# Kernel optimization log

Measured on AMD Instinct MI355X. Metric: run time of the kernel, lower is better.

Reference implementation:

```python
import jax, jax.numpy as jnp
import numpy as np

B, T, E = 2, 2048, 1024
H, D = 16, 64          # num_heads, head_dim (v_head_dim == head_dim)


def setup_inputs() -> dict:
    key = jax.random.key(0)
    ks = jax.random.split(key, 10)
    s = lambda fan_in: 1.0 / np.sqrt(fan_in)
    inp = {
        "embed": jax.random.normal(ks[0], (B, T, E), dtype=jnp.float32),
        "mask": jax.random.randint(ks[1], (B, T, T), 0, 2) > 0,
        # Linear weights stored as [in, out] (y = x @ W + b)
        "Wq": jax.random.uniform(ks[2], (E, H * D), minval=-s(E), maxval=s(E)),
        "bq": jnp.zeros((H * D,), jnp.float32),
        "Wk": jax.random.uniform(ks[3], (E, H * D), minval=-s(E), maxval=s(E)),
        "bk": jnp.zeros((H * D,), jnp.float32),
        "Wv": jax.random.uniform(ks[4], (E, H * D), minval=-s(E), maxval=s(E)),
        "bv": jnp.zeros((H * D,), jnp.float32),
        "Wz": jax.random.uniform(ks[5], (H * D, E), minval=-s(H * D), maxval=s(H * D)),
        "bz": jnp.zeros((E,), jnp.float32),
    }
    return inp


def reference(embed, mask, Wq, bq, Wk, bk, Wv, bv, Wz, bz):
    # Self-attention: context = embed
    q = (embed @ Wq + bq).reshape(B, T, H, D)   # b t h d
    k = (embed @ Wk + bk).reshape(B, T, H, D)   # b T h d
    v = (embed @ Wv + bv).reshape(B, T, H, D)   # b T h d

    scale = D ** (-0.5)
    score = jnp.einsum('bthd,bThd->bhtT', q, k) * scale   # [b,h,t,T] materialized, as in source
    max_neg = -jnp.finfo(score.dtype).max
    score = jnp.where(mask[:, None, :, :], score, max_neg)
    norm_score = jax.nn.softmax(score, axis=-1)
    z = jnp.einsum('bhtT,bThd->bthd', norm_score, v)      # [b,t,h,d]
    flat_z = z.reshape(B, T, H * D)
    return flat_z @ Wz + bz
```

## Files before the change

kernel.cpp:

```cpp
#include <hip/hip_runtime.h>
#include <hip/hip_bf16.h>


typedef __bf16 bf8_t  __attribute__((ext_vector_type(8)));
typedef __bf16 bf4_t  __attribute__((ext_vector_type(4)));
typedef float  f4_t   __attribute__((ext_vector_type(4)));

constexpr int Bb = 2, Tt = 2048, Hh = 16, Dd = 64;

#define ASYNC16(g, l)                                                        \
    __builtin_amdgcn_global_load_lds(                                        \
        (const __attribute__((address_space(1))) void*)(g),                  \
        (__attribute__((address_space(3))) void*)(l), 16, 0, 0)

#if __has_builtin(__builtin_amdgcn_exp2f)
#define EXP2F(x) __builtin_amdgcn_exp2f(x)
#else
#define EXP2F(x) exp2f(x)
#endif

__global__ __launch_bounds__(256) void prep_kernel(
    const float* __restrict__ embed, const int* __restrict__ mask,
    const float* __restrict__ w0, const float* __restrict__ w1,
    const float* __restrict__ w2, const float* __restrict__ w3,
    __bf16* __restrict__ o0, __bf16* __restrict__ o1,
    __bf16* __restrict__ o2, __bf16* __restrict__ o3,
    __bf16* __restrict__ Eb, unsigned* __restrict__ Mbits)
{
    int z = blockIdx.x;
    if (z < 4096) {
        const float* in; __bf16* out;
        switch (z >> 10) {
            case 0: in = w0; out = o0; break;
            case 1: in = w1; out = o1; break;
            case 2: in = w2; out = o2; break;
            default: in = w3; out = o3; break;
        }
        int rem = z & 1023;
        int bx = (rem & 31) * 32;
        int by = (rem >> 5) * 32;
        __shared__ float t[32][33];
        int x  = threadIdx.x & 31;
        int y0 = threadIdx.x >> 5;
        #pragma unroll
        for (int i = 0; i < 4; i++) {
            int y = y0 + i * 8;
            t[y][x] = in[(size_t)(by + y) * 1024 + bx + x];
        }
        __syncthreads();
        #pragma unroll
        for (int i = 0; i < 4; i++) {
            int y = y0 + i * 8;
            out[(size_t)(bx + y) * 1024 + by + x] = (__bf16)t[x][y];
        }
    } else if (z < 5120) {
        size_t base = (size_t)(z - 4096) * 4096;
        #pragma unroll
        for (int j = 0; j < 4; j++) {
            size_t i = base + j * 1024 + threadIdx.x * 4;
            float4 v = *reinterpret_cast<const float4*>(embed + i);
            bf4_t o = {(__bf16)v.x, (__bf16)v.y, (__bf16)v.z, (__bf16)v.w};
            *reinterpret_cast<bf4_t*>(Eb + i) = o;
        }
    } else {
        size_t g = (size_t)(z - 5120) * 256 + threadIdx.x;
        const int* mp = mask + g * 32;
        unsigned v = 0;
        #pragma unroll
        for (int i = 0; i < 8; i++) {
            int4 m4 = *reinterpret_cast<const int4*>(mp + i * 4);
            if (m4.x) v |= 1u << (i * 4 + 0);
            if (m4.y) v |= 1u << (i * 4 + 1);
            if (m4.z) v |= 1u << (i * 4 + 2);
            if (m4.w) v |= 1u << (i * 4 + 3);
        }
        Mbits[g] = v;
    }
}

template <int TM, typename OutT>
__device__ __forceinline__ void gemm_body(const __bf16* __restrict__ A,
                                          const __bf16* __restrict__ Bt,
                                          const float* __restrict__ bias,
                                          OutT* __restrict__ out,
                                          int mode, float oscale, int bx, int by)
{
    constexpr int NI = TM / 32;
    alignas(16) __shared__ __bf16 As[TM * 64];
    alignas(16) __shared__ __bf16 Bs[128 * 64];

    int tid  = threadIdx.x;
    int lane = tid & 63;
    int quad = lane >> 4;
    int l16  = lane & 15;
    int wave = tid >> 6;
    int wm   = wave >> 1, wn = wave & 1;

    f4_t acc[NI][4];
    #pragma unroll
    for (int i = 0; i < NI; i++)
        #pragma unroll
        for (int j = 0; j < 4; j++)
            acc[i][j] = f4_t{0.f, 0.f, 0.f, 0.f};

    for (int kt = 0; kt < 1024; kt += 64) {
        #pragma unroll
        for (int i = 0; i < TM / 32; i++) {
            int c   = tid + 256 * i;
            int row = c >> 3, j = c & 7;
            ASYNC16(A + (size_t)(by * TM + row) * 1024 + kt + ((j ^ (row & 7)) * 8),
                    &As[c * 8]);
        }
        #pragma unroll
        for (int i = 0; i < 4; i++) {
            int c   = tid + 256 * i;
            int row = c >> 3, j = c & 7;
            ASYNC16(Bt + (size_t)(bx * 128 + row) * 1024 + kt + ((j ^ (row & 7)) * 8),
                    &Bs[c * 8]);
        }
        __syncthreads();

        bf8_t af[2][NI], bfr[2][4];
        #pragma unroll
        for (int c = 0; c < 2; c++) {
            #pragma unroll
            for (int im = 0; im < NI; im++) {
                int row = wm * (TM / 2) + im * 16 + l16;
                af[c][im] = *reinterpret_cast<const bf8_t*>(
                    &As[row * 64 + (((c * 4 + quad) ^ (row & 7)) * 8)]);
            }
            #pragma unroll
            for (int in_ = 0; in_ < 4; in_++) {
                int row = wn * 64 + in_ * 16 + l16;
                bfr[c][in_] = *reinterpret_cast<const bf8_t*>(
                    &Bs[row * 64 + (((c * 4 + quad) ^ (row & 7)) * 8)]);
            }
        }
        #pragma unroll
        for (int c = 0; c < 2; c++)
            #pragma unroll
            for (int im = 0; im < NI; im++)
                #pragma unroll
                for (int in_ = 0; in_ < 4; in_++)
                    acc[im][in_] = __builtin_amdgcn_mfma_f32_16x16x32_bf16(
                        af[c][im], bfr[c][in_], acc[im][in_], 0, 0, 0);
        __syncthreads();
    }

    #pragma unroll
    for (int im = 0; im < NI; im++) {
        #pragma unroll
        for (int in_ = 0; in_ < 4; in_++) {
            int gc  = bx * 128 + wn * 64 + in_ * 16 + l16;
            float bb = bias[gc];
            int gr0 = by * TM + wm * (TM / 2) + im * 16 + quad * 4;
            if (mode == 2) {
                int b = gr0 >> 11, t0 = gr0 & 2047;
                int h = gc >> 6,  d = gc & 63;
                bf4_t ov;
                #pragma unroll
                for (int r = 0; r < 4; r++)
                    ov[r] = (__bf16)(acc[im][in_][r] + bb);
                *reinterpret_cast<bf4_t*>(
                    (__bf16*)out + ((size_t)(b * Hh + h) * Dd + d) * Tt + t0) = ov;
            } else {
                #pragma unroll
                for (int r = 0; r < 4; r++) {
                    int gr  = gr0 + r;
                    float v = (acc[im][in_][r] + bb) * oscale;
                    size_t idx;
                    if (mode == 0) {
                        idx = (size_t)gr * 1024 + gc;
                    } else {
                        int b = gr >> 11, t = gr & 2047;
                        int h = gc >> 6,  d = gc & 63;
                        idx = ((size_t)(b * Hh + h) * Tt + t) * Dd + d;
                    }
                    out[idx] = (OutT)v;
                }
            }
        }
    }
}

__global__ __launch_bounds__(256) void gemm_qkv_kernel(
    const __bf16* __restrict__ A,
    const __bf16* __restrict__ WqT, const __bf16* __restrict__ WkT, const __bf16* __restrict__ WvT,
    const float* __restrict__ bq,  const float* __restrict__ bk,  const float* __restrict__ bv,
    __bf16* __restrict__ Qo, __bf16* __restrict__ Ko, __bf16* __restrict__ Vo)
{
    const __bf16* Bt; const float* bias; __bf16* out; int mode; float sc;
    if      (blockIdx.z == 0) { Bt = WqT; bias = bq; out = Qo; mode = 1; sc = 0.18033688011112042f; }
    else if (blockIdx.z == 1) { Bt = WkT; bias = bk; out = Ko; mode = 1; sc = 1.f; }
    else                      { Bt = WvT; bias = bv; out = Vo; mode = 2; sc = 1.f; }
    gemm_body<128, __bf16>(A, Bt, bias, out, mode, sc, blockIdx.x, blockIdx.y);
}

__global__ __launch_bounds__(256) void gemm_out_kernel(
    const __bf16* __restrict__ A, const __bf16* __restrict__ Bt,
    const float* __restrict__ bias, float* __restrict__ out)
{
    alignas(16) __shared__ __bf16 As[64 * 64];
    alignas(16) __shared__ __bf16 Bs[64 * 64];

    int tid  = threadIdx.x;
    int lane = tid & 63;
    int quad = lane >> 4;
    int l16  = lane & 15;
    int wave = tid >> 6;
    int wm   = wave >> 1, wn = wave & 1;
    int bx = blockIdx.x, by = blockIdx.y;

    f4_t acc[2][2];
    #pragma unroll
    for (int i = 0; i < 2; i++)
        #pragma unroll
        for (int j = 0; j < 2; j++)
            acc[i][j] = f4_t{0.f, 0.f, 0.f, 0.f};

    for (int kt = 0; kt < 1024; kt += 64) {
        #pragma unroll
        for (int i = 0; i < 2; i++) {
            int c   = tid + 256 * i;
            int row = c >> 3, j = c & 7;
            ASYNC16(A + (size_t)(by * 64 + row) * 1024 + kt + ((j ^ (row & 7)) * 8),
                    &As[c * 8]);
        }
        #pragma unroll
        for (int i = 0; i < 2; i++) {
            int c   = tid + 256 * i;
            int row = c >> 3, j = c & 7;
            ASYNC16(Bt + (size_t)(bx * 64 + row) * 1024 + kt + ((j ^ (row & 7)) * 8),
                    &Bs[c * 8]);
        }
        __syncthreads();

        bf8_t af[2][2], bfr[2][2];
        #pragma unroll
        for (int c = 0; c < 2; c++) {
            #pragma unroll
            for (int im = 0; im < 2; im++) {
                int row = wm * 32 + im * 16 + l16;
                af[c][im] = *reinterpret_cast<const bf8_t*>(
                    &As[row * 64 + (((c * 4 + quad) ^ (row & 7)) * 8)]);
            }
            #pragma unroll
            for (int in_ = 0; in_ < 2; in_++) {
                int row = wn * 32 + in_ * 16 + l16;
                bfr[c][in_] = *reinterpret_cast<const bf8_t*>(
                    &Bs[row * 64 + (((c * 4 + quad) ^ (row & 7)) * 8)]);
            }
        }
        #pragma unroll
        for (int c = 0; c < 2; c++)
            #pragma unroll
            for (int im = 0; im < 2; im++)
                #pragma unroll
                for (int in_ = 0; in_ < 2; in_++)
                    acc[im][in_] = __builtin_amdgcn_mfma_f32_16x16x32_bf16(
                        af[c][im], bfr[c][in_], acc[im][in_], 0, 0, 0);
        __syncthreads();
    }

    #pragma unroll
    for (int im = 0; im < 2; im++) {
        #pragma unroll
        for (int in_ = 0; in_ < 2; in_++) {
            int gc  = bx * 64 + wn * 32 + in_ * 16 + l16;
            float bb = bias[gc];
            int gr0 = by * 64 + wm * 32 + im * 16 + quad * 4;
            #pragma unroll
            for (int r = 0; r < 4; r++)
                out[(size_t)(gr0 + r) * 1024 + gc] = acc[im][in_][r] + bb;
        }
    }
}

__global__ __launch_bounds__(512, 4) void flash_kernel(
    const __bf16* __restrict__ Qb, const __bf16* __restrict__ Kb,
    const __bf16* __restrict__ Vb, const unsigned* __restrict__ Mbits,
    __bf16* __restrict__ Zb)
{
    alignas(16) __shared__ __bf16 Ks[2][64 * 64];
    alignas(16) __shared__ __bf16 Vs[2][64 * 64];
    alignas(16) __shared__ __bf16 Ps[8 * 16 * 72];

    int tid  = threadIdx.x;
    int lane = tid & 63;
    int wave = tid >> 6;
    int quad = lane >> 4;
    int l16  = lane & 15;
    int b = blockIdx.z, h = blockIdx.y;
    int bh = b * Hh + h;
    int qrow = blockIdx.x * 128 + wave * 16;

    int srow = tid >> 3, sj = tid & 7;
    const __bf16* kgp = Kb + ((size_t)bh * Tt + srow) * Dd + ((sj ^ (srow & 7)) * 8);
    const __bf16* vgp = Vb + ((size_t)bh * Dd + srow) * Tt + ((sj ^ (srow & 7)) * 8);
    const int sdst = tid * 8;

    bf8_t qf[2];
    #pragma unroll
    for (int c = 0; c < 2; c++)
        qf[c] = *reinterpret_cast<const bf8_t*>(
            Qb + ((size_t)bh * Tt + qrow + l16) * Dd + c * 32 + quad * 8);

    bf8_t ones;
    #pragma unroll
    for (int i = 0; i < 8; i++) ones[i] = (__bf16)1.0f;

    const unsigned* bmp = Mbits + ((size_t)b * Tt + qrow + l16) * 64;

    f4_t lacc = f4_t{0.f, 0.f, 0.f, 0.f};
    f4_t o[4];
    #pragma unroll
    for (int d = 0; d < 4; d++) o[d] = f4_t{0.f, 0.f, 0.f, 0.f};

    __bf16* pw = Ps + wave * 16 * 72;

    bf8_t kreg = *reinterpret_cast<const bf8_t*>(kgp);
    bf8_t vreg = *reinterpret_cast<const bf8_t*>(vgp);
    unsigned long long mreg = *reinterpret_cast<const unsigned long long*>(bmp);

    for (int kt = 0; kt < Tt; kt += 64) {
        int par = (kt >> 6) & 1;
        *reinterpret_cast<bf8_t*>(&Ks[par][sdst]) = kreg;
        *reinterpret_cast<bf8_t*>(&Vs[par][sdst]) = vreg;
        unsigned nib[4];
        #pragma unroll
        for (int n = 0; n < 4; n++)
            nib[n] = (unsigned)(mreg >> (n * 16 + quad * 4)) & 0xFu;
        __syncthreads();

        int ktn = (kt + 64 < Tt) ? kt + 64 : 0;
        kreg = *reinterpret_cast<const bf8_t*>(kgp + (size_t)ktn * Dd);
        vreg = *reinterpret_cast<const bf8_t*>(vgp + ktn);
        mreg = *reinterpret_cast<const unsigned long long*>(bmp + (ktn >> 5));

        f4_t s[4];
        #pragma unroll
        for (int n = 0; n < 4; n++) s[n] = f4_t{0.f, 0.f, 0.f, 0.f};
        __builtin_amdgcn_s_setprio(1);
        #pragma unroll
        for (int c = 0; c < 2; c++)
            #pragma unroll
            for (int n = 0; n < 4; n++) {
                int krow = n * 16 + l16;
                bf8_t kf = *reinterpret_cast<const bf8_t*>(
                    &Ks[par][krow * 64 + (((c * 4 + quad) ^ (krow & 7)) * 8)]);
                s[n] = __builtin_amdgcn_mfma_f32_16x16x32_bf16(kf, qf[c], s[n], 0, 0, 0);
            }
        __builtin_amdgcn_s_setprio(0);

        #pragma unroll
        for (int n = 0; n < 4; n++) {
            bf4_t pv4;
            #pragma unroll
            for (int r = 0; r < 4; r++) {
                float p = (nib[n] & (1u << r)) ? EXP2F(s[n][r]) : 0.f;
                pv4[r] = (__bf16)p;
            }
            *reinterpret_cast<bf4_t*>(&pw[l16 * 72 + n * 16 + quad * 4]) = pv4;
        }

        __builtin_amdgcn_s_setprio(1);
        #pragma unroll
        for (int c = 0; c < 2; c++) {
            bf8_t pf = *reinterpret_cast<const bf8_t*>(
                &pw[l16 * 72 + c * 32 + quad * 8]);
            lacc = __builtin_amdgcn_mfma_f32_16x16x32_bf16(ones, pf, lacc, 0, 0, 0);
            #pragma unroll
            for (int ds = 0; ds < 4; ds++) {
                int vrow = ds * 16 + l16;
                bf8_t vf = *reinterpret_cast<const bf8_t*>(
                    &Vs[par][vrow * 64 + (((c * 4 + quad) ^ (vrow & 7)) * 8)]);
                o[ds] = __builtin_amdgcn_mfma_f32_16x16x32_bf16(vf, pf, o[ds], 0, 0, 0);
            }
        }
        __builtin_amdgcn_s_setprio(0);
    }

    float inv = 1.f / fmaxf(lacc[0], 1e-30f);
    size_t zrow = ((size_t)b * Tt + qrow + l16) * 1024 + h * 64;
    #pragma unroll
    for (int ds = 0; ds < 4; ds++) {
        bf4_t ov;
        #pragma unroll
        for (int r = 0; r < 4; r++) ov[r] = (__bf16)(o[ds][r] * inv);
        *reinterpret_cast<bf4_t*>(Zb + zrow + ds * 16 + quad * 4) = ov;
    }
}

extern "C" void kernel_launch(void* const* d_in, const int* in_sizes, int n_in,
                              void* d_out, int out_size, void* d_ws, size_t ws_size,
                              hipStream_t stream)
{
    (void)in_sizes; (void)n_in; (void)out_size; (void)ws_size;

    const float* embed = (const float*)d_in[0];
    const int*   mask  = (const int*)d_in[1];
    const float* Wq = (const float*)d_in[2];
    const float* bq = (const float*)d_in[3];
    const float* Wk = (const float*)d_in[4];
    const float* bk = (const float*)d_in[5];
    const float* Wv = (const float*)d_in[6];
    const float* bv = (const float*)d_in[7];
    const float* Wz = (const float*)d_in[8];
    const float* bz = (const float*)d_in[9];
    float* out = (float*)d_out;

    char* ws = (char*)d_ws;
    const size_t MB = (size_t)1024 * 1024;
    __bf16*   WqT = (__bf16*)(ws + 0 * MB);
    __bf16*   WkT = (__bf16*)(ws + 2 * MB);
    __bf16*   WvT = (__bf16*)(ws + 4 * MB);
    __bf16*   WzT = (__bf16*)(ws + 6 * MB);
    __bf16*   Eb  = (__bf16*)(ws + 8 * MB);
    __bf16*   Qb  = (__bf16*)(ws + 16 * MB);
    __bf16*   Kb  = (__bf16*)(ws + 24 * MB);
    __bf16*   Vb  = (__bf16*)(ws + 32 * MB);
    __bf16*   Zb  = (__bf16*)(ws + 40 * MB);
    unsigned* Mb  = (unsigned*)(ws + 48 * MB);

    prep_kernel<<<dim3(6144), 256, 0, stream>>>(embed, mask, Wq, Wk, Wv, Wz,
                                                WqT, WkT, WvT, WzT, Eb, Mb);
    gemm_qkv_kernel<<<dim3(8, 32, 3), 256, 0, stream>>>(Eb, WqT, WkT, WvT,
                                                        bq, bk, bv, Qb, Kb, Vb);
    flash_kernel<<<dim3(16, Hh, Bb), 512, 0, stream>>>(Qb, Kb, Vb, Mb, Zb);
    gemm_out_kernel<<<dim3(16, 64), 256, 0, stream>>>(Zb, WzT, bz, out);
}
```

Measured before the change: 225.6 us.

## Fuse Q/K/V projections into one GEMM kernel sharing A tiles, swizzle block order

```diff
diff --git a/kernel.cpp b/kernel.cpp
--- a/kernel.cpp
+++ b/kernel.cpp
@@ -78,6 +78,127 @@
     }
 }
 
+__global__ __launch_bounds__(512, 2) void gemm_qkv_fused(
+    const __bf16* __restrict__ A,
+    const __bf16* __restrict__ WqT, const __bf16* __restrict__ WkT, const __bf16* __restrict__ WvT,
+    const float* __restrict__ bq,  const float* __restrict__ bk,  const float* __restrict__ bv,
+    __bf16* __restrict__ Qo, __bf16* __restrict__ Ko, __bf16* __restrict__ Vo)
+{
+    alignas(16) __shared__ __bf16 As[128 * 64];
+    alignas(16) __shared__ __bf16 Bs[3][128 * 64];
+
+    int lin = blockIdx.x;
+    int swz = (lin & 7) * 32 + (lin >> 3);
+    int bx = swz & 7, by = swz >> 3;
+
+    int tid  = threadIdx.x;
+    int lane = tid & 63;
+    int quad = lane >> 4;
+    int l16  = lane & 15;
+    int wave = tid >> 6;
+    int wm   = wave & 3;
+    int wn   = wave >> 2;
+
+    const __bf16* Bp[3] = {WqT, WkT, WvT};
+
+    f4_t acc[3][2][4];
+    #pragma unroll
+    for (int m = 0; m < 3; m++)
+        #pragma unroll
+        for (int i = 0; i < 2; i++)
+            #pragma unroll
+            for (int j = 0; j < 4; j++)
+                acc[m][i][j] = f4_t{0.f, 0.f, 0.f, 0.f};
+
+    for (int kt = 0; kt < 1024; kt += 64) {
+        #pragma unroll
+        for (int i = 0; i < 2; i++) {
+            int c   = tid + 512 * i;
+            int row = c >> 3, j = c & 7;
+            ASYNC16(A + (size_t)(by * 128 + row) * 1024 + kt + ((j ^ (row & 7)) * 8),
+                    &As[c * 8]);
+        }
+        #pragma unroll
+        for (int m = 0; m < 3; m++)
+            #pragma unroll
+            for (int i = 0; i < 2; i++) {
+                int c   = tid + 512 * i;
+                int row = c >> 3, j = c & 7;
+                ASYNC16(Bp[m] + (size_t)(bx * 128 + row) * 1024 + kt + ((j ^ (row & 7)) * 8),
+                        &Bs[m][c * 8]);
+            }
+        __syncthreads();
+
+        bf8_t af[2][2];
+        #pragma unroll
+        for (int c = 0; c < 2; c++)
+            #pragma unroll
+            for (int im = 0; im < 2; im++) {
+                int row = wm * 32 + im * 16 + l16;
+                af[c][im] = *reinterpret_cast<const bf8_t*>(
+                    &As[row * 64 + (((c * 4 + quad) ^ (row & 7)) * 8)]);
+            }
+        #pragma unroll
+        for (int m = 0; m < 3; m++) {
+            bf8_t bfr[2][4];
+            #pragma unroll
+            for (int c = 0; c < 2; c++)
+                #pragma unroll
+                for (int in_ = 0; in_ < 4; in_++) {
+                    int row = wn * 64 + in_ * 16 + l16;
+                    bfr[c][in_] = *reinterpret_cast<const bf8_t*>(
+                        &Bs[m][row * 64 + (((c * 4 + quad) ^ (row & 7)) * 8)]);
+                }
+            #pragma unroll
+            for (int c = 0; c < 2; c++)
+                #pragma unroll
+                for (int im = 0; im < 2; im++)
+                    #pragma unroll
+                    for (int in_ = 0; in_ < 4; in_++)
+                        acc[m][im][in_] = __builtin_amdgcn_mfma_f32_16x16x32_bf16(
+                            af[c][im], bfr[c][in_], acc[m][im][in_], 0, 0, 0);
+        }
+        __syncthreads();
+    }
+
+    const float QSC = 0.18033688011112042f;
+    #pragma unroll
+    for (int im = 0; im < 2; im++) {
+        #pragma unroll
+        for (int in_ = 0; in_ < 4; in_++) {
+            int gc  = bx * 128 + wn * 64 + in_ * 16 + l16;
+            int gr0 = by * 128 + wm * 32 + im * 16 + quad * 4;
+            int b = gr0 >> 11, t0 = gr0 & 2047;
+            int h = gc >> 6,  d = gc & 63;
+            {
+                float bb = bq[gc];
+                bf4_t ov;
+                #pragma unroll
+                for (int r = 0; r < 4; r++)
+                    ov[r] = (__bf16)((acc[0][im][in_][r] + bb) * QSC);
+                *reinterpret_cast<bf4_t*>(
+                    Qo + ((size_t)(b * Hh + h) * Dd + d) * Tt + t0) = ov;
+            }
+            {
+                float bb = bk[gc];
+                #pragma unroll
+                for (int r = 0; r < 4; r++)
+                    Ko[((size_t)(b * Hh + h) * Tt + t0 + r) * Dd + d] =
+                        (__bf16)(acc[1][im][in_][r] + bb);
+            }
+            {
+                float bb = bv[gc];
+                bf4_t ov;
+                #pragma unroll
+                for (int r = 0; r < 4; r++)
+                    ov[r] = (__bf16)(acc[2][im][in_][r] + bb);
+                *reinterpret_cast<bf4_t*>(
+                    Vo + ((size_t)(b * Hh + h) * Dd + d) * Tt + t0) = ov;
+            }
+        }
+    }
+}
+
 template <int TM, typename OutT>
 __device__ __forceinline__ void gemm_body(const __bf16* __restrict__ A,
                                           const __bf16* __restrict__ Bt,
@@ -154,126 +275,24 @@
             int gc  = bx * 128 + wn * 64 + in_ * 16 + l16;
             float bb = bias[gc];
             int gr0 = by * TM + wm * (TM / 2) + im * 16 + quad * 4;
-            if (mode == 2) {
-                int b = gr0 >> 11, t0 = gr0 & 2047;
-                int h = gc >> 6,  d = gc & 63;
-                bf4_t ov;
-                #pragma unroll
-                for (int r = 0; r < 4; r++)
-                    ov[r] = (__bf16)(acc[im][in_][r] + bb);
-                *reinterpret_cast<bf4_t*>(
-                    (__bf16*)out + ((size_t)(b * Hh + h) * Dd + d) * Tt + t0) = ov;
-            } else {
-                #pragma unroll
-                for (int r = 0; r < 4; r++) {
-                    int gr  = gr0 + r;
-                    float v = (acc[im][in_][r] + bb) * oscale;
-                    size_t idx;
-                    if (mode == 0) {
-                        idx = (size_t)gr * 1024 + gc;
-                    } else {
-                        int b = gr >> 11, t = gr & 2047;
-                        int h = gc >> 6,  d = gc & 63;
-                        idx = ((size_t)(b * Hh + h) * Tt + t) * Dd + d;
-                    }
-                    out[idx] = (OutT)v;
-                }
-            }
-        }
-    }
-}
-
-__global__ __launch_bounds__(256) void gemm_qkv_kernel(
-    const __bf16* __restrict__ A,
-    const __bf16* __restrict__ WqT, const __bf16* __restrict__ WkT, const __bf16* __restrict__ WvT,
-    const float* __restrict__ bq,  const float* __restrict__ bk,  const float* __restrict__ bv,
-    __bf16* __restrict__ Qo, __bf16* __restrict__ Ko, __bf16* __restrict__ Vo)
-{
-    const __bf16* Bt; const float* bias; __bf16* out; int mode; float sc;
-    if      (blockIdx.z == 0) { Bt = WqT; bias = bq; out = Qo; mode = 1; sc = 0.18033688011112042f; }
-    else if (blockIdx.z == 1) { Bt = WkT; bias = bk; out = Ko; mode = 1; sc = 1.f; }
-    else                      { Bt = WvT; bias = bv; out = Vo; mode = 2; sc = 1.f; }
-    gemm_body<128, __bf16>(A, Bt, bias, out, mode, sc, blockIdx.x, blockIdx.y);
+            #pragma unroll
+            for (int r = 0; r < 4; r++) {
+                int gr  = gr0 + r;
+                float v = (acc[im][in_][r] + bb) * oscale;
+                out[(size_t)gr * 1024 + gc] = (OutT)v;
+            }
+        }
+    }
+    (void)mode;
 }
 
 __global__ __launch_bounds__(256) void gemm_out_kernel(
     const __bf16* __restrict__ A, const __bf16* __restrict__ Bt,
     const float* __restrict__ bias, float* __restrict__ out)
 {
-    alignas(16) __shared__ __bf16 As[64 * 64];
-    alignas(16) __shared__ __bf16 Bs[64 * 64];
-
-    int tid  = threadIdx.x;
-    int lane = tid & 63;
-    int quad = lane >> 4;
-    int l16  = lane & 15;
-    int wave = tid >> 6;
-    int wm   = wave >> 1, wn = wave & 1;
-    int bx = blockIdx.x, by = blockIdx.y;
-
-    f4_t acc[2][2];
-    #pragma unroll
-    for (int i = 0; i < 2; i++)
-        #pragma unroll
-        for (int j = 0; j < 2; j++)
-            acc[i][j] = f4_t{0.f, 0.f, 0.f, 0.f};
-
-    for (int kt = 0; kt < 1024; kt += 64) {
-        #pragma unroll
-        for (int i = 0; i < 2; i++) {
-            int c   = tid + 256 * i;
-            int row = c >> 3, j = c & 7;
-            ASYNC16(A + (size_t)(by * 64 + row) * 1024 + kt + ((j ^ (row & 7)) * 8),
-                    &As[c * 8]);
-        }
-        #pragma unroll
-        for (int i = 0; i < 2; i++) {
-            int c   = tid + 256 * i;
-            int row = c >> 3, j = c & 7;
-            ASYNC16(Bt + (size_t)(bx * 64 + row) * 1024 + kt + ((j ^ (row & 7)) * 8),
-                    &Bs[c * 8]);
-        }
-        __syncthreads();
-
-        bf8_t af[2][2], bfr[2][2];
-        #pragma unroll
-        for (int c = 0; c < 2; c++) {
-            #pragma unroll
-            for (int im = 0; im < 2; im++) {
-                int row = wm * 32 + im * 16 + l16;
-                af[c][im] = *reinterpret_cast<const bf8_t*>(
-                    &As[row * 64 + (((c * 4 + quad) ^ (row & 7)) * 8)]);
-            }
-            #pragma unroll
-            for (int in_ = 0; in_ < 2; in_++) {
-                int row = wn * 32 + in_ * 16 + l16;
-                bfr[c][in_] = *reinterpret_cast<const bf8_t*>(
-                    &Bs[row * 64 + (((c * 4 + quad) ^ (row & 7)) * 8)]);
-            }
-        }
-        #pragma unroll
-        for (int c = 0; c < 2; c++)
-            #pragma unroll
-            for (int im = 0; im < 2; im++)
-                #pragma unroll
-                for (int in_ = 0; in_ < 2; in_++)
-                    acc[im][in_] = __builtin_amdgcn_mfma_f32_16x16x32_bf16(
-                        af[c][im], bfr[c][in_], acc[im][in_], 0, 0, 0);
-        __syncthreads();
-    }
-
-    #pragma unroll
-    for (int im = 0; im < 2; im++) {
-        #pragma unroll
-        for (int in_ = 0; in_ < 2; in_++) {
-            int gc  = bx * 64 + wn * 32 + in_ * 16 + l16;
-            float bb = bias[gc];
-            int gr0 = by * 64 + wm * 32 + im * 16 + quad * 4;
-            #pragma unroll
-            for (int r = 0; r < 4; r++)
-                out[(size_t)(gr0 + r) * 1024 + gc] = acc[im][in_][r] + bb;
-        }
-    }
+    int lin = blockIdx.x + 8 * blockIdx.y;
+    int swz = (lin & 7) * 64 + (lin >> 3);
+    gemm_body<64, float>(A, Bt, bias, out, 0, 1.f, swz & 7, swz >> 3);
 }
 
 __global__ __launch_bounds__(512, 4) void flash_kernel(
@@ -302,8 +321,10 @@
     bf8_t qf[2];
     #pragma unroll
     for (int c = 0; c < 2; c++)
-        qf[c] = *reinterpret_cast<const bf8_t*>(
-            Qb + ((size_t)bh * Tt + qrow + l16) * Dd + c * 32 + quad * 8);
+        #pragma unroll
+        for (int j = 0; j < 8; j++)
+            qf[c][j] = Qb[((size_t)bh * Dd + c * 32 + quad * 8 + j) * Tt
+                          + qrow + l16];
 
     bf8_t ones;
     #pragma unroll
@@ -424,8 +445,8 @@
 
     prep_kernel<<<dim3(6144), 256, 0, stream>>>(embed, mask, Wq, Wk, Wv, Wz,
                                                 WqT, WkT, WvT, WzT, Eb, Mb);
-    gemm_qkv_kernel<<<dim3(8, 32, 3), 256, 0, stream>>>(Eb, WqT, WkT, WvT,
-                                                        bq, bk, bv, Qb, Kb, Vb);
+    gemm_qkv_fused<<<dim3(256), 512, 0, stream>>>(Eb, WqT, WkT, WvT,
+                                                  bq, bk, bv, Qb, Kb, Vb);
     flash_kernel<<<dim3(16, Hh, Bb), 512, 0, stream>>>(Qb, Kb, Vb, Mb, Zb);
-    gemm_out_kernel<<<dim3(16, 64), 256, 0, stream>>>(Zb, WzT, bz, out);
-}
+    gemm_out_kernel<<<dim3(8, 64), 256, 0, stream>>>(Zb, WzT, bz, out);
+}
```

Result: no change. 223.0 us (-1.2%).
